# Kernel tuning notes

Hardware: AMD Instinct MI355X
Metric: run time of the kernel (lower is better)

The kernel has to match this reference:

```python
import jax, jax.numpy as jnp
import numpy as np

B, T, F, H1, H2 = 8192, 50, 25, 200, 100


def setup_inputs() -> dict:
    key = jax.random.key(0)
    ks = jax.random.split(key, 16)
    s1 = 1.0 / np.sqrt(H1)
    s2 = 1.0 / np.sqrt(H2)
    return {
        "x": jax.random.normal(ks[0], (B, T, F), jnp.float32),
        "W_ih1": jax.random.normal(ks[1], (4 * H1, F), jnp.float32) * s1,
        "W_hh1": jax.random.normal(ks[2], (4 * H1, H1), jnp.float32) * s1,
        "b_ih1": jax.random.normal(ks[3], (4 * H1,), jnp.float32) * s1,
        "b_hh1": jax.random.normal(ks[4], (4 * H1,), jnp.float32) * s1,
        "W_ih2": jax.random.normal(ks[5], (4 * H2, H1), jnp.float32) * s2,
        "W_hh2": jax.random.normal(ks[6], (4 * H2, H2), jnp.float32) * s2,
        "b_ih2": jax.random.normal(ks[7], (4 * H2,), jnp.float32) * s2,
        "b_hh2": jax.random.normal(ks[8], (4 * H2,), jnp.float32) * s2,
        "fc_w": jax.random.normal(ks[9], (1, H2), jnp.float32) * s2,
        "fc_b": jax.random.normal(ks[10], (1,), jnp.float32) * s2,
        # torch.rand -> uniform [0,1)
        "h1_0": jax.random.uniform(ks[11], (B, H1), jnp.float32),
        "c1_0": jax.random.uniform(ks[12], (B, H1), jnp.float32),
        "h2_0": jax.random.uniform(ks[13], (B, H2), jnp.float32),
        "c2_0": jax.random.uniform(ks[14], (B, H2), jnp.float32),
    }


def _lstm_cell(pre_x, h, c, W_hh):
    # pre_x: x_t @ W_ih.T + b_ih + b_hh (precomputed). PyTorch gate order i,f,g,o.
    gates = pre_x + h @ W_hh.T
    i, f, g, o = jnp.split(gates, 4, axis=-1)
    i = jax.nn.sigmoid(i)
    f = jax.nn.sigmoid(f)
    g = jnp.tanh(g)
    o = jax.nn.sigmoid(o)
    c = f * c + i * g
    h = o * jnp.tanh(c)
    return h, c


def reference(x, W_ih1, W_hh1, b_ih1, b_hh1, W_ih2, W_hh2, b_ih2, b_hh2,
              fc_w, fc_b, h1_0, c1_0, h2_0, c2_0):
    b = x.shape[0]
    xs = jnp.transpose(x.reshape(b, T, F), (1, 0, 2))  # [T, B, F]
    pre1 = jnp.einsum("tbf,gf->tbg", xs, W_ih1) + (b_ih1 + b_hh1)  # [T, B, 4H1]

    def step(carry, pre_t):
        h, c = carry
        h, c = _lstm_cell(pre_t, h, c, W_hh1)
        return (h, c), h

    _, out1 = jax.lax.scan(step, (h1_0, c1_0), pre1)  # [T, B, H1]

    # NOTE: the original loop writes `out2, hidden = self.LSTM2(..., hidden2)`,
    # so hidden2 is NEVER updated: every layer-2 step uses the same initial
    # (h2_0, c2_0), and only the LAST timestep's output is used downstream.
    x_last = out1[-1]  # [B, H1]
    pre2 = x_last @ W_ih2.T + (b_ih2 + b_hh2)
    h2, _ = _lstm_cell(pre2, h2_0, c2_0, W_hh2)  # [B, H2]

    return jax.nn.sigmoid(h2 @ fc_w.T + fc_b)  # [B, 1]
```

## Files before the change

kernel.cpp:

```cpp
#include <hip/hip_runtime.h>
#include <hip/hip_bf16.h>

#define BTOT 8192
#define TSTEPS 50
#define FIN 25
#define H1C 200
#define G1C 800
#define H2C 100
#define KPAD 256
#define BM 32
#define AST 264

typedef __bf16 bf16_t;
typedef __bf16 bf16x8 __attribute__((ext_vector_type(8)));
typedef float f32x16 __attribute__((ext_vector_type(16)));

__device__ __forceinline__ float sigm(float x) {
  float e = __builtin_amdgcn_exp2f(-1.4426950408889634f * x);
  return __builtin_amdgcn_rcpf(1.0f + e);
}
__device__ __forceinline__ float tanha(float x) {
  float e = __builtin_amdgcn_exp2f(-2.885390081777927f * x);
  return 2.0f * __builtin_amdgcn_rcpf(1.0f + e) - 1.0f;
}

__global__ void prep_kernel(const float* __restrict__ Wih1, const float* __restrict__ Whh1,
                            const float* __restrict__ bih1, const float* __restrict__ bhh1,
                            bf16_t* __restrict__ Wcat, float* __restrict__ bcat) {
  int tid = blockIdx.x * blockDim.x + threadIdx.x;
  for (int e = tid; e < G1C * KPAD; e += gridDim.x * blockDim.x) {
    int n = e >> 8, k = e & 255;
    int nt = n >> 5, local = n & 31;
    int u = nt * 8 + (local >> 2);
    int gate = local & 3;
    int orig = gate * 200 + u;
    float v = 0.f;
    if (k < 200) v = Whh1[orig * 200 + k];
    else if (k < 225) v = Wih1[orig * 25 + (k - 200)];
    Wcat[e] = (bf16_t)v;
  }
  if (tid < G1C) {
    int n = tid;
    int nt = n >> 5, local = n & 31;
    int u = nt * 8 + (local >> 2);
    int gate = local & 3;
    int orig = gate * 200 + u;
    bcat[n] = bih1[orig] + bhh1[orig];
  }
}

__global__ __launch_bounds__(512, 2) void lstm_main(
    const float* __restrict__ x,
    const bf16_t* __restrict__ Wcat, const float* __restrict__ bcat,
    const float* __restrict__ h10, const float* __restrict__ c10,
    const float* __restrict__ Wih2, const float* __restrict__ Whh2,
    const float* __restrict__ bih2, const float* __restrict__ bhh2,
    const float* __restrict__ fcw, const float* __restrict__ fcb,
    const float* __restrict__ h20, const float* __restrict__ c20,
    float* __restrict__ out) {

  __shared__ __align__(16) bf16_t As[2][BM * AST];
  __shared__ float h2s[BM * 101];
  __shared__ float c2s[BM * 101];
  __shared__ float facc[BM];

  const int tid = threadIdx.x;
  const int lane = tid & 63;
  const int wid = tid >> 6;
  const int gbase = blockIdx.x * BM;

  const int tstart = (wid == 0) ? 0 : (1 + 3 * wid);
  const int tcnt = (wid == 0) ? 4 : 3;

  const int l31 = lane & 31;
  const int h5 = lane >> 5;
  const int p = lane & 3;
  const int uq = l31 >> 2;

  for (int i = tid; i < 2 * BM * AST; i += 512) ((bf16_t*)As)[i] = (bf16_t)0.f;
  __syncthreads();
  for (int i = tid; i < BM * H1C; i += 512) {
    int r = i / H1C, u = i - r * H1C;
    As[0][r * AST + u] = (bf16_t)h10[(gbase + r) * H1C + u];
  }
  for (int i = tid; i < BM * FIN; i += 512) {
    int r = i / FIN, f = i - r * FIN;
    As[0][r * AST + 200 + f] = (bf16_t)x[(size_t)(gbase + r) * (TSTEPS * FIN) + f];
  }

  float bv[4];
  float cc[16];
  #pragma unroll
  for (int nt = 0; nt < 4; ++nt) {
    bv[nt] = 0.f;
    #pragma unroll
    for (int i = 0; i < 4; ++i) cc[nt * 4 + i] = 0.f;
    if (nt < tcnt) {
      bv[nt] = bcat[(tstart + nt) * 32 + l31];
      int u = (tstart + nt) * 8 + uq;
      #pragma unroll
      for (int i = 0; i < 4; ++i) {
        int r = 8 * p + 4 * h5 + i;
        cc[nt * 4 + i] = c10[(gbase + r) * H1C + u];
      }
    }
  }

  unsigned xg[2], xl[2]; bool xv[2];
  #pragma unroll
  for (int j = 0; j < 2; ++j) {
    int i = tid + 512 * j;
    xv[j] = (i < BM * FIN);
    int r = i / FIN; if (r > BM - 1) r = BM - 1;
    int f = i - (i / FIN) * FIN;
    xg[j] = (unsigned)(gbase + r) * (TSTEPS * FIN) + f;
    xl[j] = (unsigned)(r * AST + 200 + f);
  }
  __syncthreads();

  const bf16x8* __restrict__ Wv = (const bf16x8*)Wcat;

  bf16x8 bA[16], bB[16];
  int pb = 0;
  {
    const bf16x8* wp = Wv + ((tstart * 32 + l31) * 32 + h5);
    #pragma unroll
    for (int kt = 0; kt < 16; ++kt) bA[kt] = wp[kt * 2];
  }

  #pragma unroll 1
  for (int t = 0; t < TSTEPS; ++t) {
    const bf16_t* __restrict__ Ac = As[t & 1];
    bf16_t* __restrict__ An = As[(t & 1) ^ 1];

    float xr[2] = {0.f, 0.f};
    if (t < TSTEPS - 1) {
      #pragma unroll
      for (int j = 0; j < 2; ++j) if (xv[j]) xr[j] = x[xg[j] + (unsigned)(t + 1) * FIN];
    }

    #pragma unroll
    for (int nt = 0; nt < 4; ++nt) {
      if (nt < tcnt) {
        int ptile = (nt + 1 < tcnt) ? (tstart + nt + 1) : tstart;
        const bf16x8* wp = Wv + ((ptile * 32 + l31) * 32 + h5);

        f32x16 A;
        #pragma unroll
        for (int q = 0; q < 16; ++q) A[q] = bv[nt];

        if (pb == 0) {
          #pragma unroll
          for (int kt = 0; kt < 16; ++kt) bB[kt] = wp[kt * 2];
          #pragma unroll
          for (int kt = 0; kt < 16; ++kt) {
            bf16x8 a = *(const bf16x8*)(&Ac[l31 * AST + kt * 16 + h5 * 8]);
            A = __builtin_amdgcn_mfma_f32_32x32x16_bf16(a, bA[kt], A, 0, 0, 0);
          }
        } else {
          #pragma unroll
          for (int kt = 0; kt < 16; ++kt) bA[kt] = wp[kt * 2];
          #pragma unroll
          for (int kt = 0; kt < 16; ++kt) {
            bf16x8 a = *(const bf16x8*)(&Ac[l31 * AST + kt * 16 + h5 * 8]);
            A = __builtin_amdgcn_mfma_f32_32x32x16_bf16(a, bB[kt], A, 0, 0, 0);
          }
        }
        pb ^= 1;

        int u = (tstart + nt) * 8 + uq;
        #pragma unroll
        for (int i = 0; i < 4; ++i) {
          float s0 = A[i], s1 = A[4 + i], s2 = A[8 + i], s3 = A[12 + i];
          float own = (p == 0) ? s0 : (p == 1) ? s1 : (p == 2) ? s2 : s3;
          int q1 = p ^ 1;
          float t1 = (q1 == 0) ? s0 : (q1 == 1) ? s1 : (q1 == 2) ? s2 : s3;
          float r1 = __shfl_xor(t1, 1);
          int q2 = p ^ 2;
          float t2 = (q2 == 0) ? s0 : (q2 == 1) ? s1 : (q2 == 2) ? s2 : s3;
          float r2 = __shfl_xor(t2, 2);
          int q3 = p ^ 3;
          float t3 = (q3 == 0) ? s0 : (q3 == 1) ? s1 : (q3 == 2) ? s2 : s3;
          float r3 = __shfl_xor(t3, 3);
          float vi = (p == 0) ? own : (p == 1) ? r1 : (p == 2) ? r2 : r3;
          float vf = (p == 0) ? r1 : (p == 1) ? own : (p == 2) ? r3 : r2;
          float vg = (p == 0) ? r2 : (p == 1) ? r3 : (p == 2) ? own : r1;
          float vo = (p == 0) ? r3 : (p == 1) ? r2 : (p == 2) ? r1 : own;
          float ig = sigm(vi), fg = sigm(vf), gg = tanha(vg), og = sigm(vo);
          float cn = fg * cc[nt * 4 + i] + ig * gg;
          cc[nt * 4 + i] = cn;
          float hv = og * tanha(cn);
          int r = 8 * p + 4 * h5 + i;
          An[r * AST + u] = (bf16_t)hv;
        }
      }
    }

    if (t < TSTEPS - 1) {
      #pragma unroll
      for (int j = 0; j < 2; ++j) if (xv[j]) An[xl[j]] = (bf16_t)xr[j];
    }
    __syncthreads();
  }

  const bf16_t* __restrict__ hf = As[0];

  for (int i = tid; i < BM * H2C; i += 512) {
    int r = i / H2C, u = i - r * H2C;
    h2s[r * 101 + u] = h20[(gbase + r) * H2C + u];
    c2s[r * 101 + u] = c20[(gbase + r) * H2C + u];
  }
  if (tid < BM) facc[tid] = 0.f;
  __syncthreads();

  const float fcb0 = fcb[0];
  for (int i = tid; i < BM * H2C; i += 512) {
    int u = i >> 5;
    int r = i & 31;
    float a0 = bih2[u] + bhh2[u];
    float a1 = bih2[100 + u] + bhh2[100 + u];
    float a2 = bih2[200 + u] + bhh2[200 + u];
    float a3 = bih2[300 + u] + bhh2[300 + u];
    const float4* w0 = (const float4*)(Wih2 + (0 * H2C + u) * H1C);
    const float4* w1 = (const float4*)(Wih2 + (1 * H2C + u) * H1C);
    const float4* w2 = (const float4*)(Wih2 + (2 * H2C + u) * H1C);
    const float4* w3 = (const float4*)(Wih2 + (3 * H2C + u) * H1C);
    #pragma unroll 5
    for (int k4 = 0; k4 < 50; ++k4) {
      float hk0 = (float)hf[r * AST + 4 * k4 + 0];
      float hk1 = (float)hf[r * AST + 4 * k4 + 1];
      float hk2 = (float)hf[r * AST + 4 * k4 + 2];
      float hk3 = (float)hf[r * AST + 4 * k4 + 3];
      float4 wv;
      wv = w0[k4]; a0 += hk0 * wv.x + hk1 * wv.y + hk2 * wv.z + hk3 * wv.w;
      wv = w1[k4]; a1 += hk0 * wv.x + hk1 * wv.y + hk2 * wv.z + hk3 * wv.w;
      wv = w2[k4]; a2 += hk0 * wv.x + hk1 * wv.y + hk2 * wv.z + hk3 * wv.w;
      wv = w3[k4]; a3 += hk0 * wv.x + hk1 * wv.y + hk2 * wv.z + hk3 * wv.w;
    }
    const float4* v0 = (const float4*)(Whh2 + (0 * H2C + u) * H2C);
    const float4* v1 = (const float4*)(Whh2 + (1 * H2C + u) * H2C);
    const float4* v2 = (const float4*)(Whh2 + (2 * H2C + u) * H2C);
    const float4* v3 = (const float4*)(Whh2 + (3 * H2C + u) * H2C);
    #pragma unroll 5
    for (int k4 = 0; k4 < 25; ++k4) {
      float hk0 = h2s[r * 101 + 4 * k4 + 0];
      float hk1 = h2s[r * 101 + 4 * k4 + 1];
      float hk2 = h2s[r * 101 + 4 * k4 + 2];
      float hk3 = h2s[r * 101 + 4 * k4 + 3];
      float4 wv;
      wv = v0[k4]; a0 += hk0 * wv.x + hk1 * wv.y + hk2 * wv.z + hk3 * wv.w;
      wv = v1[k4]; a1 += hk0 * wv.x + hk1 * wv.y + hk2 * wv.z + hk3 * wv.w;
      wv = v2[k4]; a2 += hk0 * wv.x + hk1 * wv.y + hk2 * wv.z + hk3 * wv.w;
      wv = v3[k4]; a3 += hk0 * wv.x + hk1 * wv.y + hk2 * wv.z + hk3 * wv.w;
    }
    float ig = sigm(a0), fg = sigm(a1), gg = tanha(a2), og = sigm(a3);
    float cn = fg * c2s[r * 101 + u] + ig * gg;
    float h2v = og * tanha(cn);
    atomicAdd(&facc[r], h2v * fcw[u]);
  }
  __syncthreads();
  if (tid < BM) out[gbase + tid] = sigm(facc[tid] + fcb0);
}

extern "C" void kernel_launch(void* const* d_in, const int* in_sizes, int n_in,
                              void* d_out, int out_size, void* d_ws, size_t ws_size,
                              hipStream_t stream) {
  const float* x    = (const float*)d_in[0];
  const float* Wih1 = (const float*)d_in[1];
  const float* Whh1 = (const float*)d_in[2];
  const float* bih1 = (const float*)d_in[3];
  const float* bhh1 = (const float*)d_in[4];
  const float* Wih2 = (const float*)d_in[5];
  const float* Whh2 = (const float*)d_in[6];
  const float* bih2 = (const float*)d_in[7];
  const float* bhh2 = (const float*)d_in[8];
  const float* fcw  = (const float*)d_in[9];
  const float* fcb  = (const float*)d_in[10];
  const float* h10  = (const float*)d_in[11];
  const float* c10  = (const float*)d_in[12];
  const float* h20  = (const float*)d_in[13];
  const float* c20  = (const float*)d_in[14];
  float* out = (float*)d_out;

  bf16_t* Wcat = (bf16_t*)d_ws;
  float* bcat = (float*)((char*)d_ws + (size_t)G1C * KPAD * sizeof(bf16_t));

  prep_kernel<<<256, 256, 0, stream>>>(Wih1, Whh1, bih1, bhh1, Wcat, bcat);
  lstm_main<<<BTOT / BM, 512, 0, stream>>>(x, Wcat, bcat, h10, c10,
                                           Wih2, Whh2, bih2, bhh2,
                                           fcw, fcb, h20, c20, out);
}
```

Before: 1.053 ms.

## Use 16 waves per block, fewer tiles per wave, and coalesced weight layout

Doubles the block to 1024 threads so each wave handles one or two 32-gate tiles instead of three or four, which shortens the per-step serial chain inside a block. The packed weight layout is reordered so each wave's B-fragment loads for a k-step are contiguous across lanes. The double-buffered weight registers are replaced by a single buffer that is refilled right after the MFMAs. The costs are higher register pressure under launch_bounds(1024,4) and more waves contending at each per-step barrier.

```diff
diff --git a/kernel.cpp b/kernel.cpp
--- a/kernel.cpp
+++ b/kernel.cpp
@@ -10,6 +10,7 @@
 #define KPAD 256
 #define BM 32
 #define AST 264
+#define TSTRIDE 1024
 
 typedef __bf16 bf16_t;
 typedef __bf16 bf16x8 __attribute__((ext_vector_type(8)));
@@ -29,10 +30,14 @@
                             bf16_t* __restrict__ Wcat, float* __restrict__ bcat) {
   int tid = blockIdx.x * blockDim.x + threadIdx.x;
   for (int e = tid; e < G1C * KPAD; e += gridDim.x * blockDim.x) {
-    int n = e >> 8, k = e & 255;
-    int nt = n >> 5, local = n & 31;
-    int u = nt * 8 + (local >> 2);
-    int gate = local & 3;
+    int elem = e & 7;
+    int h5p = (e >> 3) & 1;
+    int l31p = (e >> 4) & 31;
+    int kt = (e >> 9) & 15;
+    int tile = e >> 13;
+    int k = kt * 16 + h5p * 8 + elem;
+    int u = tile * 8 + (l31p >> 2);
+    int gate = l31p & 3;
     int orig = gate * 200 + u;
     float v = 0.f;
     if (k < 200) v = Whh1[orig * 200 + k];
@@ -41,15 +46,60 @@
   }
   if (tid < G1C) {
     int n = tid;
-    int nt = n >> 5, local = n & 31;
-    int u = nt * 8 + (local >> 2);
+    int tile = n >> 5, local = n & 31;
+    int u = tile * 8 + (local >> 2);
     int gate = local & 3;
     int orig = gate * 200 + u;
     bcat[n] = bih1[orig] + bhh1[orig];
   }
 }
 
-__global__ __launch_bounds__(512, 2) void lstm_main(
+__device__ __forceinline__ void proc_tile(
+    const bf16_t* __restrict__ Ac, bf16_t* __restrict__ An,
+    const bf16x8* __restrict__ Wv, bf16x8 (&b)[16],
+    int this_tile, int next_tile, float bvv, float* cc,
+    int l31, int h5, int p, int uq) {
+  f32x16 A;
+  #pragma unroll
+  for (int q = 0; q < 16; ++q) A[q] = bvv;
+  #pragma unroll
+  for (int kt = 0; kt < 16; ++kt) {
+    bf16x8 a = *(const bf16x8*)(&Ac[l31 * AST + kt * 16 + h5 * 8]);
+    A = __builtin_amdgcn_mfma_f32_32x32x16_bf16(a, b[kt], A, 0, 0, 0);
+  }
+  {
+    const bf16x8* wp = Wv + next_tile * TSTRIDE + (l31 * 2 + h5);
+    #pragma unroll
+    for (int kt = 0; kt < 16; ++kt) b[kt] = wp[kt * 64];
+  }
+  int u = this_tile * 8 + uq;
+  #pragma unroll
+  for (int i = 0; i < 4; ++i) {
+    float s0 = A[i], s1 = A[4 + i], s2 = A[8 + i], s3 = A[12 + i];
+    float own = (p == 0) ? s0 : (p == 1) ? s1 : (p == 2) ? s2 : s3;
+    int q1 = p ^ 1;
+    float t1 = (q1 == 0) ? s0 : (q1 == 1) ? s1 : (q1 == 2) ? s2 : s3;
+    float r1 = __shfl_xor(t1, 1);
+    int q2 = p ^ 2;
+    float t2 = (q2 == 0) ? s0 : (q2 == 1) ? s1 : (q2 == 2) ? s2 : s3;
+    float r2 = __shfl_xor(t2, 2);
+    int q3 = p ^ 3;
+    float t3 = (q3 == 0) ? s0 : (q3 == 1) ? s1 : (q3 == 2) ? s2 : s3;
+    float r3 = __shfl_xor(t3, 3);
+    float vi = (p == 0) ? own : (p == 1) ? r1 : (p == 2) ? r2 : r3;
+    float vf = (p == 0) ? r1 : (p == 1) ? own : (p == 2) ? r3 : r2;
+    float vg = (p == 0) ? r2 : (p == 1) ? r3 : (p == 2) ? own : r1;
+    float vo = (p == 0) ? r3 : (p == 1) ? r2 : (p == 2) ? r1 : own;
+    float ig = sigm(vi), fg = sigm(vf), gg = tanha(vg), og = sigm(vo);
+    float cn = fg * cc[i] + ig * gg;
+    cc[i] = cn;
+    float hv = og * tanha(cn);
+    int r = 8 * p + 4 * h5 + i;
+    An[r * AST + u] = (bf16_t)hv;
+  }
+}
+
+__global__ __launch_bounds__(1024, 4) void lstm_main(
     const float* __restrict__ x,
     const bf16_t* __restrict__ Wcat, const float* __restrict__ bcat,
     const float* __restrict__ h10, const float* __restrict__ c10,
@@ -69,29 +119,29 @@
   const int wid = tid >> 6;
   const int gbase = blockIdx.x * BM;
 
-  const int tstart = (wid == 0) ? 0 : (1 + 3 * wid);
-  const int tcnt = (wid == 0) ? 4 : 3;
+  const int tcnt = (wid < 9) ? 2 : 1;
+  const int tstart = (wid < 9) ? 2 * wid : wid + 9;
 
   const int l31 = lane & 31;
   const int h5 = lane >> 5;
   const int p = lane & 3;
   const int uq = l31 >> 2;
 
-  for (int i = tid; i < 2 * BM * AST; i += 512) ((bf16_t*)As)[i] = (bf16_t)0.f;
-  __syncthreads();
-  for (int i = tid; i < BM * H1C; i += 512) {
+  for (int i = tid; i < 2 * BM * AST; i += 1024) ((bf16_t*)As)[i] = (bf16_t)0.f;
+  __syncthreads();
+  for (int i = tid; i < BM * H1C; i += 1024) {
     int r = i / H1C, u = i - r * H1C;
     As[0][r * AST + u] = (bf16_t)h10[(gbase + r) * H1C + u];
   }
-  for (int i = tid; i < BM * FIN; i += 512) {
-    int r = i / FIN, f = i - r * FIN;
+  if (tid < BM * FIN) {
+    int r = tid / FIN, f = tid - (tid / FIN) * FIN;
     As[0][r * AST + 200 + f] = (bf16_t)x[(size_t)(gbase + r) * (TSTEPS * FIN) + f];
   }
 
-  float bv[4];
-  float cc[16];
-  #pragma unroll
-  for (int nt = 0; nt < 4; ++nt) {
+  float bv[2];
+  float cc[8];
+  #pragma unroll
+  for (int nt = 0; nt < 2; ++nt) {
     bv[nt] = 0.f;
     #pragma unroll
     for (int i = 0; i < 4; ++i) cc[nt * 4 + i] = 0.f;
@@ -106,26 +156,22 @@
     }
   }
 
-  unsigned xg[2], xl[2]; bool xv[2];
-  #pragma unroll
-  for (int j = 0; j < 2; ++j) {
-    int i = tid + 512 * j;
-    xv[j] = (i < BM * FIN);
-    int r = i / FIN; if (r > BM - 1) r = BM - 1;
-    int f = i - (i / FIN) * FIN;
-    xg[j] = (unsigned)(gbase + r) * (TSTEPS * FIN) + f;
-    xl[j] = (unsigned)(r * AST + 200 + f);
+  const bool xvld = (tid < BM * FIN);
+  unsigned xg = 0, xlo = 0;
+  if (xvld) {
+    int r = tid / FIN, f = tid - (tid / FIN) * FIN;
+    xg = (unsigned)(gbase + r) * (TSTEPS * FIN) + f;
+    xlo = (unsigned)(r * AST + 200 + f);
   }
   __syncthreads();
 
   const bf16x8* __restrict__ Wv = (const bf16x8*)Wcat;
 
-  bf16x8 bA[16], bB[16];
-  int pb = 0;
+  bf16x8 b[16];
   {
-    const bf16x8* wp = Wv + ((tstart * 32 + l31) * 32 + h5);
+    const bf16x8* wp = Wv + tstart * TSTRIDE + (l31 * 2 + h5);
     #pragma unroll
-    for (int kt = 0; kt < 16; ++kt) bA[kt] = wp[kt * 2];
+    for (int kt = 0; kt < 16; ++kt) b[kt] = wp[kt * 64];
   }
 
   #pragma unroll 1
@@ -133,79 +179,22 @@
     const bf16_t* __restrict__ Ac = As[t & 1];
     bf16_t* __restrict__ An = As[(t & 1) ^ 1];
 
-    float xr[2] = {0.f, 0.f};
-    if (t < TSTEPS - 1) {
-      #pragma unroll
-      for (int j = 0; j < 2; ++j) if (xv[j]) xr[j] = x[xg[j] + (unsigned)(t + 1) * FIN];
-    }
-
-    #pragma unroll
-    for (int nt = 0; nt < 4; ++nt) {
-      if (nt < tcnt) {
-        int ptile = (nt + 1 < tcnt) ? (tstart + nt + 1) : tstart;
-        const bf16x8* wp = Wv + ((ptile * 32 + l31) * 32 + h5);
-
-        f32x16 A;
-        #pragma unroll
-        for (int q = 0; q < 16; ++q) A[q] = bv[nt];
-
-        if (pb == 0) {
-          #pragma unroll
-          for (int kt = 0; kt < 16; ++kt) bB[kt] = wp[kt * 2];
-          #pragma unroll
-          for (int kt = 0; kt < 16; ++kt) {
-            bf16x8 a = *(const bf16x8*)(&Ac[l31 * AST + kt * 16 + h5 * 8]);
-            A = __builtin_amdgcn_mfma_f32_32x32x16_bf16(a, bA[kt], A, 0, 0, 0);
-          }
-        } else {
-          #pragma unroll
-          for (int kt = 0; kt < 16; ++kt) bA[kt] = wp[kt * 2];
-          #pragma unroll
-          for (int kt = 0; kt < 16; ++kt) {
-            bf16x8 a = *(const bf16x8*)(&Ac[l31 * AST + kt * 16 + h5 * 8]);
-            A = __builtin_amdgcn_mfma_f32_32x32x16_bf16(a, bB[kt], A, 0, 0, 0);
-          }
-        }
-        pb ^= 1;
-
-        int u = (tstart + nt) * 8 + uq;
-        #pragma unroll
-        for (int i = 0; i < 4; ++i) {
-          float s0 = A[i], s1 = A[4 + i], s2 = A[8 + i], s3 = A[12 + i];
-          float own = (p == 0) ? s0 : (p == 1) ? s1 : (p == 2) ? s2 : s3;
-          int q1 = p ^ 1;
-          float t1 = (q1 == 0) ? s0 : (q1 == 1) ? s1 : (q1 == 2) ? s2 : s3;
-          float r1 = __shfl_xor(t1, 1);
-          int q2 = p ^ 2;
-          float t2 = (q2 == 0) ? s0 : (q2 == 1) ? s1 : (q2 == 2) ? s2 : s3;
-          float r2 = __shfl_xor(t2, 2);
-          int q3 = p ^ 3;
-          float t3 = (q3 == 0) ? s0 : (q3 == 1) ? s1 : (q3 == 2) ? s2 : s3;
-          float r3 = __shfl_xor(t3, 3);
-          float vi = (p == 0) ? own : (p == 1) ? r1 : (p == 2) ? r2 : r3;
-          float vf = (p == 0) ? r1 : (p == 1) ? own : (p == 2) ? r3 : r2;
-          float vg = (p == 0) ? r2 : (p == 1) ? r3 : (p == 2) ? own : r1;
-          float vo = (p == 0) ? r3 : (p == 1) ? r2 : (p == 2) ? r1 : own;
-          float ig = sigm(vi), fg = sigm(vf), gg = tanha(vg), og = sigm(vo);
-          float cn = fg * cc[nt * 4 + i] + ig * gg;
-          cc[nt * 4 + i] = cn;
-          float hv = og * tanha(cn);
-          int r = 8 * p + 4 * h5 + i;
-          An[r * AST + u] = (bf16_t)hv;
-        }
-      }
-    }
-
-    if (t < TSTEPS - 1) {
-      #pragma unroll
-      for (int j = 0; j < 2; ++j) if (xv[j]) An[xl[j]] = (bf16_t)xr[j];
-    }
+    float xr = 0.f;
+    if (t < TSTEPS - 1 && xvld) xr = x[xg + (unsigned)(t + 1) * FIN];
+
+    proc_tile(Ac, An, Wv, b, tstart, (tcnt == 2) ? tstart + 1 : tstart,
+              bv[0], cc + 0, l31, h5, p, uq);
+    if (tcnt == 2)
+      proc_tile(Ac, An, Wv, b, tstart + 1, tstart,
+                bv[1], cc + 4, l31, h5, p, uq);
+
+    if (t < TSTEPS - 1 && xvld) An[xlo] = (bf16_t)xr;
     __syncthreads();
   }
 
   const bf16_t* __restrict__ hf = As[0];
 
-  for (int i = tid; i < BM * H2C; i += 512) {
+  for (int i = tid; i < BM * H2C; i += 1024) {
     int r = i / H2C, u = i - r * H2C;
     h2s[r * 101 + u] = h20[(gbase + r) * H2C + u];
     c2s[r * 101 + u] = c20[(gbase + r) * H2C + u];
@@ -214,7 +203,7 @@
   __syncthreads();
 
   const float fcb0 = fcb[0];
-  for (int i = tid; i < BM * H2C; i += 512) {
+  for (int i = tid; i < BM * H2C; i += 1024) {
     int u = i >> 5;
     int r = i & 31;
     float a0 = bih2[u] + bhh2[u];
@@ -286,7 +275,7 @@
   float* bcat = (float*)((char*)d_ws + (size_t)G1C * KPAD * sizeof(bf16_t));
 
   prep_kernel<<<256, 256, 0, stream>>>(Wih1, Whh1, bih1, bhh1, Wcat, bcat);
-  lstm_main<<<BTOT / BM, 512, 0, stream>>>(x, Wcat, bcat, h10, c10,
-                                           Wih2, Whh2, bih2, bhh2,
-                                           fcw, fcb, h20, c20, out);
-}
+  lstm_main<<<BTOT / BM, 1024, 0, stream>>>(x, Wcat, bcat, h10, c10,
+                                            Wih2, Whh2, bih2, bhh2,
+                                            fcw, fcb, h20, c20, out);
+}
```

New measurement: 1.355 ms. +28.7%, slower.
